# Kernel optimization log

Measured on AMD Instinct MI355X. Metric: run time of the kernel, lower is better.

## Reference

```python
import jax, jax.numpy as jnp
import numpy as np

REG1 = 0.5
REG2 = 0.5
ALPHA = 0.5

def setup_inputs() -> dict:
    key = jax.random.key(0)
    k1, k2, k3, k4, k5 = jax.random.split(key, 5)
    N, D, K = 32768, 256, 2048
    return {
        "encoder_out": jax.random.normal(k1, (N, D), dtype=jnp.float32),
        "prototypes": jax.random.normal(k2, (K, D), dtype=jnp.float32),
        "recon_loss": jax.random.uniform(k3, (), dtype=jnp.float32),
        "kl_loss": jax.random.uniform(k4, (), dtype=jnp.float32),
        "mmd_loss": jax.random.uniform(k5, (), dtype=jnp.float32),
    }


def _cdist_min_loss(z, prototypes):
    # torch.cdist(z, protos) -> [N, K]; f_dist = cdist(protos, z) = its transpose.
    # prototypes accessed via .data in torch -> detached.
    p = jax.lax.stop_gradient(prototypes)
    z2 = jnp.sum(z * z, axis=1, keepdims=True)          # [N, 1]
    p2 = jnp.sum(p * p, axis=1)                          # [K]
    sq = z2 + p2[None, :] - 2.0 * (z @ p.T)              # [N, K]
    dist = jnp.sqrt(jnp.maximum(sq, 0.0))
    p_min = jnp.min(dist, axis=1).mean()   # p_dist.min(1).values.mean()
    f_min = jnp.min(dist, axis=0).mean()   # f_dist [K,N].min(1) == dist.min(0)
    return REG1 * p_min + REG2 * f_min


def reference(encoder_out, prototypes, recon_loss, kl_loss, mmd_loss):
    cvae_loss = recon_loss + ALPHA * kl_loss + mmd_loss
    prot_decoding_loss = _cdist_min_loss(encoder_out, prototypes)
    # no projection head (use_projector=False)
    x = encoder_out / jnp.maximum(
        jnp.linalg.norm(encoder_out, axis=1, keepdims=True), 1e-12)
    x_mapped = x @ prototypes.T  # [N, K]
    return (encoder_out, x, x_mapped, cvae_loss, prot_decoding_loss)
```

## Files before the change

kernel.cpp:

```cpp
#include <hip/hip_runtime.h>
#include <hip/hip_bf16.h>

typedef __bf16 bf16x8 __attribute__((ext_vector_type(8)));
typedef __bf16 bf16x4 __attribute__((ext_vector_type(4)));
typedef float  f32x4  __attribute__((ext_vector_type(4)));

#define N_ROWS 32768
#define D_DIM  256
#define K_PROT 2048

#define WS_Z2    0
#define WS_INVN  32768
#define WS_P2    65536
#define WS_ACC   67584
#define WS_RP    67600
#define WS_CP    (67600 + 524288)
#define WS_ZB    (67600 + 1048576)
#define WS_PB    (67600 + 1048576 + 4194304)

#define OUT_X0   0UL
#define OUT_X1   8388608UL
#define OUT_XMAP 16777216UL
#define OUT_CVAE 83886080UL
#define OUT_PROT 83886081UL

__device__ __forceinline__ void gload16(const __bf16* gsrc, const __bf16* ldst) {
    auto g = (const __attribute__((address_space(1))) unsigned int*)(unsigned long long)gsrc;
    auto l = (__attribute__((address_space(3))) unsigned int*)(unsigned long long)ldst;
    __builtin_amdgcn_global_load_lds(g, l, 16, 0, 0);
}

__global__ __launch_bounds__(256) void k12_rows(
    const float* __restrict__ Z, const float* __restrict__ P,
    float* __restrict__ out0, float* __restrict__ out1,
    float* __restrict__ z2, float* __restrict__ invn,
    __bf16* __restrict__ Zb,
    float* __restrict__ p2, __bf16* __restrict__ Pb,
    float* __restrict__ accw)
{
    int b    = blockIdx.x;
    int lane = threadIdx.x & 63;
    if (b == 0 && threadIdx.x < 2) accw[threadIdx.x] = 0.0f;
    if (b < (N_ROWS/4)) {
        int row  = (b << 2) + (threadIdx.x >> 6);
        size_t base = (size_t)row * D_DIM;
        float4 v = ((const float4*)(Z + base))[lane];
        float ss = v.x*v.x + v.y*v.y + v.z*v.z + v.w*v.w;
        #pragma unroll
        for (int d = 32; d >= 1; d >>= 1) ss += __shfl_xor(ss, d);
        float inv = 1.0f / fmaxf(sqrtf(ss), 1e-12f);
        ((float4*)(out0 + base))[lane] = v;
        float4 xv; xv.x = v.x*inv; xv.y = v.y*inv; xv.z = v.z*inv; xv.w = v.w*inv;
        ((float4*)(out1 + base))[lane] = xv;
        bf16x4 bv; bv[0]=(__bf16)v.x; bv[1]=(__bf16)v.y; bv[2]=(__bf16)v.z; bv[3]=(__bf16)v.w;
        ((bf16x4*)(Zb + base))[lane] = bv;
        if (lane == 0) { z2[row] = ss; invn[row] = inv; }
    } else {
        int row  = ((b - (N_ROWS/4)) << 2) + (threadIdx.x >> 6);
        size_t base = (size_t)row * D_DIM;
        float4 v = ((const float4*)(P + base))[lane];
        float ss = v.x*v.x + v.y*v.y + v.z*v.z + v.w*v.w;
        #pragma unroll
        for (int d = 32; d >= 1; d >>= 1) ss += __shfl_xor(ss, d);
        bf16x4 bv; bv[0]=(__bf16)v.x; bv[1]=(__bf16)v.y; bv[2]=(__bf16)v.z; bv[3]=(__bf16)v.w;
        ((bf16x4*)(Pb + base))[lane] = bv;
        if (lane == 0) { p2[row] = ss; }
    }
}

#define BM 128
#define BN 128
#define BK 64

__global__ __launch_bounds__(256, 3) void k3_gemm(
    const __bf16* __restrict__ Zb, const __bf16* __restrict__ Pb,
    const float* __restrict__ z2, const float* __restrict__ p2,
    const float* __restrict__ invn,
    float* __restrict__ xmap,
    float* __restrict__ rp, float* __restrict__ cp)
{
    __shared__ __bf16 As[BM * BK];
    __shared__ __bf16 Bs[BN * BK];

    const int tid  = threadIdx.x;
    const int wg   = (blockIdx.x & 7) * 512 + (blockIdx.x >> 3);
    const int bn   = wg & 15;
    const int bm   = wg >> 4;
    const int lane = tid & 63;
    const int wave = tid >> 6;
    const int wm   = wave >> 1;
    const int wn   = wave & 1;
    const int l15  = lane & 15;
    const int quad = lane >> 4;

    const int m0 = bm * BM;
    const int n0 = bn * BN;

    f32x4 acc[4][4];
    #pragma unroll
    for (int i = 0; i < 4; i++)
        #pragma unroll
        for (int j = 0; j < 4; j++)
            #pragma unroll
            for (int r = 0; r < 4; r++) acc[i][j][r] = 0.0f;

    const int ch_row[4] = {
        ((0*4 + wave)*64 + lane) >> 3, ((1*4 + wave)*64 + lane) >> 3,
        ((2*4 + wave)*64 + lane) >> 3, ((3*4 + wave)*64 + lane) >> 3 };
    const int ch_c = lane & 7;

    for (int kt = 0; kt < D_DIM; kt += BK) {
        #pragma unroll
        for (int it = 0; it < 4; it++) {
            const __bf16* aS = Zb + (size_t)(m0 + ch_row[it]) * D_DIM + kt + ch_c * 8;
            const __bf16* bS = Pb + (size_t)(n0 + ch_row[it]) * D_DIM + kt + ch_c * 8;
            gload16(aS, As + (it*4 + wave) * 512);
            gload16(bS, Bs + (it*4 + wave) * 512);
        }
        __syncthreads();

        #pragma unroll
        for (int s = 0; s < 2; s++) {
            bf16x8 af[4], bfr[4];
            #pragma unroll
            for (int i = 0; i < 4; i++)
                af[i] = *(const bf16x8*)(As + (wm*64 + i*16 + l15) * BK + s*32 + quad*8);
            #pragma unroll
            for (int j = 0; j < 4; j++)
                bfr[j] = *(const bf16x8*)(Bs + (wn*64 + j*16 + l15) * BK + s*32 + quad*8);
            #pragma unroll
            for (int i = 0; i < 4; i++)
                #pragma unroll
                for (int j = 0; j < 4; j++)
                    acc[i][j] = __builtin_amdgcn_mfma_f32_16x16x32_bf16(af[i], bfr[j], acc[i][j], 0, 0, 0);
        }
        __syncthreads();
    }

    float invr[16], zzr[16];
    #pragma unroll
    for (int i = 0; i < 4; i++)
        #pragma unroll
        for (int r = 0; r < 4; r++) {
            int gm = m0 + wm*64 + i*16 + quad*4 + r;
            invr[i*4+r] = invn[gm];
            zzr[i*4+r]  = z2[gm];
        }
    float pp[4];
    #pragma unroll
    for (int j = 0; j < 4; j++) pp[j] = p2[n0 + wn*64 + j*16 + l15];

    float cminv[4] = {3.0e38f, 3.0e38f, 3.0e38f, 3.0e38f};
    float rvv[16];

    #pragma unroll
    for (int i = 0; i < 4; i++) {
        #pragma unroll
        for (int r = 0; r < 4; r++) {
            int gm = m0 + wm*64 + i*16 + quad*4 + r;
            float zi = zzr[i*4+r], iv = invr[i*4+r];
            size_t orow = (size_t)gm * K_PROT + n0 + wn*64 + l15;
            float rv = 3.0e38f;
            #pragma unroll
            for (int j = 0; j < 4; j++) {
                float g = acc[i][j][r];
                xmap[orow + j*16] = g * iv;
                float d2 = fmaxf(zi + pp[j] - 2.0f*g, 0.0f);
                rv = fminf(rv, d2);
                cminv[j] = fminf(cminv[j], d2);
            }
            #pragma unroll
            for (int s = 1; s < 16; s <<= 1) rv = fminf(rv, __shfl_xor(rv, s));
            rvv[i*4+r] = rv;
        }
    }
    float cvv[4];
    #pragma unroll
    for (int j = 0; j < 4; j++) {
        float cv = cminv[j];
        cv = fminf(cv, __shfl_xor(cv, 16));
        cv = fminf(cv, __shfl_xor(cv, 32));
        cvv[j] = cv;
    }

    float* srow = (float*)As;
    float* scol = srow + 128;
    if (wn == 0 && l15 == 0) {
        #pragma unroll
        for (int i = 0; i < 4; i++)
            #pragma unroll
            for (int r = 0; r < 4; r++)
                srow[wm*64 + i*16 + quad*4 + r] = rvv[i*4+r];
    }
    if (wm == 0 && quad == 0) {
        #pragma unroll
        for (int j = 0; j < 4; j++) scol[wn*64 + j*16 + l15] = cvv[j];
    }
    __syncthreads();
    if (wn == 1 && l15 == 0) {
        #pragma unroll
        for (int i = 0; i < 4; i++)
            #pragma unroll
            for (int r = 0; r < 4; r++) {
                int idx = wm*64 + i*16 + quad*4 + r;
                srow[idx] = fminf(srow[idx], rvv[i*4+r]);
            }
    }
    if (wm == 1 && quad == 0) {
        #pragma unroll
        for (int j = 0; j < 4; j++) {
            int c = wn*64 + j*16 + l15;
            scol[c] = fminf(scol[c], cvv[j]);
        }
    }
    __syncthreads();
    if (tid < 128)       rp[(size_t)bn * N_ROWS + m0 + tid] = srow[tid];
    else if (tid < 256)  cp[(size_t)bm * K_PROT + n0 + (tid - 128)] = scol[tid - 128];
}

__global__ __launch_bounds__(256) void k4_reduce(
    const float* __restrict__ rp, const float* __restrict__ cp,
    float* __restrict__ accw)
{
    __shared__ float sbuf[160];
    int b = blockIdx.x, t = threadIdx.x;
    int lane = t & 63, w = t >> 6;
    if (b < 64) {
        float a = 0.0f;
        #pragma unroll
        for (int rr = 0; rr < 2; rr++) {
            int row = b*512 + rr*256 + t;
            float m = 3.0e38f;
            #pragma unroll
            for (int k = 0; k < 16; k++) m = fminf(m, rp[(size_t)k * N_ROWS + row]);
            a += sqrtf(m);
        }
        #pragma unroll
        for (int d = 32; d >= 1; d >>= 1) a += __shfl_xor(a, d);
        if (lane == 0) sbuf[w] = a;
        __syncthreads();
        if (t == 0) atomicAdd(accw + 0, sbuf[0] + sbuf[1] + sbuf[2] + sbuf[3]);
    } else {
        int col  = (b - 64) * 128 + (t & 127);
        int half = t >> 7;
        float m = 3.0e38f;
        for (int k = half*128; k < half*128 + 128; k++)
            m = fminf(m, cp[(size_t)k * K_PROT + col]);
        if (half == 0) sbuf[t] = m;
        __syncthreads();
        if (half == 1) sbuf[t - 128] = fminf(sbuf[t - 128], m);
        __syncthreads();
        if (t < 128) {
            float s = sqrtf(sbuf[t]);
            #pragma unroll
            for (int d = 32; d >= 1; d >>= 1) s += __shfl_xor(s, d);
            if (lane == 0) sbuf[128 + (t >> 6)] = s;
        }
        __syncthreads();
        if (t == 0) atomicAdd(accw + 1, sbuf[128] + sbuf[129]);
    }
}

__global__ void k5_final(
    const float* __restrict__ accw,
    const float* __restrict__ recon, const float* __restrict__ kl,
    const float* __restrict__ mmd, float* __restrict__ out)
{
    out[OUT_CVAE] = recon[0] + 0.5f*kl[0] + mmd[0];
    out[OUT_PROT] = 0.5f*(accw[0] / (float)N_ROWS) + 0.5f*(accw[1] / (float)K_PROT);
}

extern "C" void kernel_launch(void* const* d_in, const int* in_sizes, int n_in,
                              void* d_out, int out_size, void* d_ws, size_t ws_size,
                              hipStream_t stream)
{
    const float* Z     = (const float*)d_in[0];
    const float* P     = (const float*)d_in[1];
    const float* recon = (const float*)d_in[2];
    const float* kl    = (const float*)d_in[3];
    const float* mmd   = (const float*)d_in[4];
    float* out = (float*)d_out;
    float* ws  = (float*)d_ws;

    float* z2   = ws + WS_Z2;
    float* invn = ws + WS_INVN;
    float* p2   = ws + WS_P2;
    float* accw = ws + WS_ACC;
    float* rp   = ws + WS_RP;
    float* cp   = ws + WS_CP;
    __bf16* Zb = (__bf16*)(ws + WS_ZB);
    __bf16* Pb = (__bf16*)(ws + WS_PB);

    hipLaunchKernelGGL(k12_rows, dim3(N_ROWS/4 + K_PROT/4), dim3(256), 0, stream,
                       Z, P, out + OUT_X0, out + OUT_X1, z2, invn, Zb, p2, Pb, accw);
    hipLaunchKernelGGL(k3_gemm, dim3((N_ROWS/BM)*(K_PROT/BN)), dim3(256), 0, stream,
                       Zb, Pb, z2, p2, invn, out + OUT_XMAP, rp, cp);
    hipLaunchKernelGGL(k4_reduce, dim3(80), dim3(256), 0, stream, rp, cp, accw);
    hipLaunchKernelGGL(k5_final, dim3(1), dim3(1), 0, stream, accw, recon, kl, mmd, out);
}
```

Baseline: 432.7 us.

## Double-buffer GEMM K-loop and stage xmap stores through LDS for vector writes

New measurement: 450.4 us. +4.1%, slower.

```diff
diff --git a/kernel.cpp b/kernel.cpp
--- a/kernel.cpp
+++ b/kernel.cpp
@@ -72,15 +72,15 @@
 #define BN 128
 #define BK 64
 
-__global__ __launch_bounds__(256, 3) void k3_gemm(
+__global__ __launch_bounds__(256, 2) void k3_gemm(
     const __bf16* __restrict__ Zb, const __bf16* __restrict__ Pb,
     const float* __restrict__ z2, const float* __restrict__ p2,
     const float* __restrict__ invn,
     float* __restrict__ xmap,
     float* __restrict__ rp, float* __restrict__ cp)
 {
-    __shared__ __bf16 As[BM * BK];
-    __shared__ __bf16 Bs[BN * BK];
+    __shared__ __bf16 As[2][BM * BK];
+    __shared__ __bf16 Bs[2][BN * BK];
 
     const int tid  = threadIdx.x;
     const int wg   = (blockIdx.x & 7) * 512 + (blockIdx.x >> 3);
@@ -109,33 +109,46 @@
         ((2*4 + wave)*64 + lane) >> 3, ((3*4 + wave)*64 + lane) >> 3 };
     const int ch_c = lane & 7;
 
-    for (int kt = 0; kt < D_DIM; kt += BK) {
-        #pragma unroll
-        for (int it = 0; it < 4; it++) {
-            const __bf16* aS = Zb + (size_t)(m0 + ch_row[it]) * D_DIM + kt + ch_c * 8;
-            const __bf16* bS = Pb + (size_t)(n0 + ch_row[it]) * D_DIM + kt + ch_c * 8;
-            gload16(aS, As + (it*4 + wave) * 512);
-            gload16(bS, Bs + (it*4 + wave) * 512);
-        }
-        __syncthreads();
-
+    #define STAGE(buf, kt)                                                            \
+        {                                                                             \
+            _Pragma("unroll")                                                         \
+            for (int it = 0; it < 4; it++) {                                          \
+                const __bf16* aS = Zb + (size_t)(m0 + ch_row[it]) * D_DIM + (kt) + ch_c * 8; \
+                const __bf16* bS = Pb + (size_t)(n0 + ch_row[it]) * D_DIM + (kt) + ch_c * 8; \
+                gload16(aS, As[buf] + (it*4 + wave) * 512);                           \
+                gload16(bS, Bs[buf] + (it*4 + wave) * 512);                           \
+            }                                                                         \
+        }
+
+    STAGE(0, 0);
+    __syncthreads();
+
+    #pragma unroll
+    for (int t = 0; t < 4; t++) {
+        const int cur = t & 1;
+        if (t + 1 < 4) STAGE(cur ^ 1, (t + 1) * BK);
+
+        bf16x8 af[2][4], bfr[2][4];
         #pragma unroll
         for (int s = 0; s < 2; s++) {
-            bf16x8 af[4], bfr[4];
             #pragma unroll
             for (int i = 0; i < 4; i++)
-                af[i] = *(const bf16x8*)(As + (wm*64 + i*16 + l15) * BK + s*32 + quad*8);
+                af[s][i] = *(const bf16x8*)(As[cur] + (wm*64 + i*16 + l15) * BK + s*32 + quad*8);
             #pragma unroll
             for (int j = 0; j < 4; j++)
-                bfr[j] = *(const bf16x8*)(Bs + (wn*64 + j*16 + l15) * BK + s*32 + quad*8);
+                bfr[s][j] = *(const bf16x8*)(Bs[cur] + (wn*64 + j*16 + l15) * BK + s*32 + quad*8);
+        }
+        #pragma unroll
+        for (int s = 0; s < 2; s++)
             #pragma unroll
             for (int i = 0; i < 4; i++)
                 #pragma unroll
                 for (int j = 0; j < 4; j++)
-                    acc[i][j] = __builtin_amdgcn_mfma_f32_16x16x32_bf16(af[i], bfr[j], acc[i][j], 0, 0, 0);
-        }
-        __syncthreads();
-    }
+                    acc[i][j] = __builtin_amdgcn_mfma_f32_16x16x32_bf16(af[s][i], bfr[s][j], acc[i][j], 0, 0, 0);
+
+        __syncthreads();
+    }
+    #undef STAGE
 
     float invr[16], zzr[16];
     #pragma unroll
@@ -157,14 +170,11 @@
     for (int i = 0; i < 4; i++) {
         #pragma unroll
         for (int r = 0; r < 4; r++) {
-            int gm = m0 + wm*64 + i*16 + quad*4 + r;
-            float zi = zzr[i*4+r], iv = invr[i*4+r];
-            size_t orow = (size_t)gm * K_PROT + n0 + wn*64 + l15;
+            float zi = zzr[i*4+r];
             float rv = 3.0e38f;
             #pragma unroll
             for (int j = 0; j < 4; j++) {
                 float g = acc[i][j][r];
-                xmap[orow + j*16] = g * iv;
                 float d2 = fmaxf(zi + pp[j] - 2.0f*g, 0.0f);
                 rv = fminf(rv, d2);
                 cminv[j] = fminf(cminv[j], d2);
@@ -183,7 +193,30 @@
         cvv[j] = cv;
     }
 
-    float* srow = (float*)As;
+    {
+        float* ep = ((float*)As) + wave * 1024;
+        #pragma unroll
+        for (int i = 0; i < 4; i++) {
+            #pragma unroll
+            for (int r = 0; r < 4; r++) {
+                float iv = invr[i*4+r];
+                #pragma unroll
+                for (int j = 0; j < 4; j++) {
+                    int widx = ((quad*4 + r)*64 + j*16 + l15) ^ (quad << 3);
+                    ep[widx] = acc[i][j][r] * iv;
+                }
+            }
+            #pragma unroll
+            for (int p = 0; p < 4; p++) {
+                int ridx = (p*256 + (lane>>4)*64 + (lane&15)*4) ^ (p << 3);
+                f32x4 vv = *(const f32x4*)(ep + ridx);
+                int grow = m0 + wm*64 + i*16 + p*4 + (lane>>4);
+                *(f32x4*)(xmap + (size_t)grow * K_PROT + n0 + wn*64 + (lane&15)*4) = vv;
+            }
+        }
+    }
+
+    float* srow = (float*)Bs;
     float* scol = srow + 128;
     if (wn == 0 && l15 == 0) {
         #pragma unroll
```
